# Performance work log

Hardware: AMD Instinct MI355X
Metric: run time of the kernel (lower is better)

The kernel has to match this reference:

```python
import jax, jax.numpy as jnp
import numpy as np

N_NODES = 50000
N_EDGES = 800000
F_IN, F_HID, F_OUT = 128, 256, 10


def setup_inputs() -> dict:
    key = jax.random.key(0)
    ks = jax.random.split(key, 8)
    x = jax.random.normal(ks[0], (N_NODES, F_IN), dtype=jnp.float32)
    edge_index = jax.random.randint(ks[1], (2, N_EDGES), 0, N_NODES, dtype=jnp.int64)
    # Glorot-ish init for GCNConv weights (PyG GCNConv: lin weight [in,out] + bias [out])
    def glorot(k, fi, fo):
        s = (6.0 / (fi + fo)) ** 0.5
        return jax.random.uniform(k, (fi, fo), minval=-s, maxval=s, dtype=jnp.float32)
    return {
        "x": x,
        "edge_index": edge_index,
        "W1": glorot(ks[2], F_IN, F_HID), "b1": jnp.zeros((F_HID,), jnp.float32),
        "W2": glorot(ks[3], F_HID, F_HID), "b2": jnp.zeros((F_HID,), jnp.float32),
        "W3": glorot(ks[4], F_HID, F_OUT), "b3": jnp.zeros((F_OUT,), jnp.float32),
    }


def _gcn_conv(x, W, b, src, dst, norm, n_nodes):
    # GCNConv: out[dst] += norm_e * (x @ W)[src]; then + bias
    xw = x @ W                                   # [N, F_out]
    msgs = norm[:, None] * xw[src]               # [E+N, F_out] gather
    agg = jax.ops.segment_sum(msgs, dst, num_segments=n_nodes)
    return agg + b


def reference(x, edge_index, W1, b1, W2, b2, W3, b3):
    n = x.shape[0]
    loops = jnp.arange(n, dtype=edge_index.dtype)
    src = jnp.concatenate([edge_index[0], loops])  # source nodes (messages from)
    dst = jnp.concatenate([edge_index[1], loops])  # target nodes (aggregate into)
    # symmetric normalization D^{-1/2} (A+I) D^{-1/2}, degree from target index
    deg = jax.ops.segment_sum(jnp.ones_like(dst, dtype=x.dtype), dst, num_segments=n)
    dinv = jnp.where(deg > 0, jax.lax.rsqrt(deg), 0.0)
    norm = dinv[src] * dinv[dst]

    h = _gcn_conv(x, W1, b1, src, dst, norm, n)
    h = jax.nn.relu(h)                  # dropout is identity in eval mode
    h = _gcn_conv(h, W2, b2, src, dst, norm, n)
    h = jax.nn.relu(h)
    h = _gcn_conv(h, W3, b3, src, dst, norm, n)
    return jax.nn.log_softmax(h, axis=1)
```

## Files before the change

kernel.cpp:

```cpp
#include <hip/hip_runtime.h>
#include <hip/hip_bf16.h>
#include <math.h>

#define F_IN 128
#define F_HID 256
#define F_OUT 10

typedef __attribute__((ext_vector_type(4))) short s16x4;
typedef __attribute__((ext_vector_type(8))) short s16x8;
typedef __attribute__((ext_vector_type(4))) float f32x4;

static __device__ __forceinline__ float b2f(unsigned short u) {
    union { float f; unsigned int u; } c;
    c.u = ((unsigned int)u) << 16;
    return c.f;
}
static __device__ __forceinline__ unsigned short f2b(float f) {
    return __bfloat16_as_ushort(__float2bfloat16(f));
}


__global__ void prep_kernel(const int* __restrict__ dst, int* __restrict__ cnt, int e,
                            const float* __restrict__ x, unsigned short* __restrict__ xb,
                            int xq,
                            const float* __restrict__ W1, unsigned short* __restrict__ W1t,
                            const float* __restrict__ W2, unsigned short* __restrict__ W2t) {
    int i = blockIdx.x * blockDim.x + threadIdx.x;
    int job = blockIdx.y;
    if (job == 0) {
        if (i < e) atomicAdd(&cnt[dst[i]], 1);
    } else if (job == 1) {
        if (i < xq) {
            float4 v = *(const float4*)&x[(size_t)i * 4];
            ushort4 o;
            o.x = f2b(v.x); o.y = f2b(v.y); o.z = f2b(v.z); o.w = f2b(v.w);
            *(ushort4*)&xb[(size_t)i * 4] = o;
        }
    } else if (job == 2) {
        if (i < F_IN * F_HID) {
            int k = i / F_HID, nn = i - k * F_HID;
            W1t[nn * F_IN + k] = f2b(W1[i]);
        }
    } else {
        if (i < F_HID * F_HID) {
            int k = i / F_HID, nn = i - k * F_HID;
            W2t[nn * F_HID + k] = f2b(W2[i]);
        }
    }
}


__global__ void scan1_kernel(const int* __restrict__ cnt, int* __restrict__ rowstart,
                             int* __restrict__ partial, float* __restrict__ dinv, int n) {
    __shared__ int s[256];
    int tid = threadIdx.x;
    int i = blockIdx.x * 256 + tid;
    int v = (i < n) ? cnt[i] : 0;
    s[tid] = v;
    __syncthreads();
    for (int off = 1; off < 256; off <<= 1) {
        int t = (tid >= off) ? s[tid - off] : 0;
        __syncthreads();
        s[tid] += t;
        __syncthreads();
    }
    if (i < n) {
        rowstart[i] = s[tid] - v;
        dinv[i] = rsqrtf((float)(v + 1));
    }
    if (tid == 255) partial[blockIdx.x] = s[255];
}

__global__ void scan2_kernel(int* __restrict__ partial, int nb) {
    __shared__ int s[256];
    int tid = threadIdx.x;
    int v = (tid < nb) ? partial[tid] : 0;
    s[tid] = v;
    __syncthreads();
    for (int off = 1; off < 256; off <<= 1) {
        int t = (tid >= off) ? s[tid - off] : 0;
        __syncthreads();
        s[tid] += t;
        __syncthreads();
    }
    if (tid < nb) partial[tid] = s[tid] - v;
}

__global__ void scan3_kernel(int* __restrict__ rowstart, const int* __restrict__ partial,
                             int n, int e) {
    int i = blockIdx.x * blockDim.x + threadIdx.x;
    if (i < n) rowstart[i] += partial[blockIdx.x];
    if (i == 0) rowstart[n] = e;
}

__global__ void fill_kernel(const int* __restrict__ src, const int* __restrict__ dst,
                            const int* __restrict__ rowstart, int* __restrict__ cursor,
                            const float* __restrict__ dinv, int2* __restrict__ pack, int e) {
    int i = blockIdx.x * blockDim.x + threadIdx.x;
    if (i >= e) return;
    int s = src[i], d = dst[i];
    int pos = rowstart[d] + atomicAdd(&cursor[d], 1);
    float w = dinv[s] * dinv[d];
    pack[pos] = make_int2(s, __float_as_int(w));
}


template <int F>
__global__ __launch_bounds__(256) void agg_kernel(const unsigned short* __restrict__ feat,
                                                  const int* __restrict__ rowstart,
                                                  const int2* __restrict__ pack,
                                                  const float* __restrict__ dinv,
                                                  unsigned short* __restrict__ out, int n) {
    constexpr int LPF = F / 8;
    constexpr int EG = 64 / LPF;
    int wid = threadIdx.x >> 6;
    int lane = threadIdx.x & 63;
    int v = blockIdx.x * 4 + wid;
    if (v >= n) return;
    int eg = lane / LPF;
    int fl = lane % LPF;
    const unsigned short* fp = feat + fl * 8;

    float acc[8];
    {
        float d = dinv[v];
        float sw = (eg == 0) ? d * d : 0.f;
        s16x8 t = *(const s16x8*)&fp[(size_t)v * F];
#pragma unroll
        for (int j = 0; j < 8; ++j) acc[j] = sw * b2f((unsigned short)t[j]);
    }

    int e0 = rowstart[v], e1 = rowstart[v + 1];
    constexpr int STEP = EG * 4;
    int e = e0;
    for (; e + STEP <= e1; e += STEP) {
        int2 p[4];
#pragma unroll
        for (int u = 0; u < 4; ++u) p[u] = pack[e + eg + u * EG];
        s16x8 t[4];
#pragma unroll
        for (int u = 0; u < 4; ++u) t[u] = *(const s16x8*)&fp[(size_t)p[u].x * F];
#pragma unroll
        for (int u = 0; u < 4; ++u) {
            float w = __int_as_float(p[u].y);
#pragma unroll
            for (int j = 0; j < 8; ++j) acc[j] += w * b2f((unsigned short)t[u][j]);
        }
    }
    for (int ee = e + eg; ee < e1; ee += EG) {
        int2 p = pack[ee];
        float w = __int_as_float(p.y);
        s16x8 t = *(const s16x8*)&fp[(size_t)p.x * F];
#pragma unroll
        for (int j = 0; j < 8; ++j) acc[j] += w * b2f((unsigned short)t[j]);
    }

    if (EG == 4) {
#pragma unroll
        for (int j = 0; j < 8; ++j) acc[j] += __shfl_xor(acc[j], 16);
    }
#pragma unroll
    for (int j = 0; j < 8; ++j) acc[j] += __shfl_xor(acc[j], 32);

    if (eg == 0) {
        s16x8 o;
#pragma unroll
        for (int j = 0; j < 8; ++j) o[j] = (short)f2b(acc[j]);
        *(s16x8*)&out[(size_t)v * F + fl * 8] = o;
    }
}


template <int K, bool RELU, bool BF16OUT>
__global__ __launch_bounds__(256) void gemm_mfma_kernel(const unsigned short* __restrict__ A,
                                                        const unsigned short* __restrict__ Bt,
                                                        const float* __restrict__ bias,
                                                        float* __restrict__ C,
                                                        unsigned short* __restrict__ Cb,
                                                        int M, int N) {
    __shared__ unsigned short As[64][40];
    __shared__ unsigned short Bs[64][40];
    int tid = threadIdx.x;
    int w = tid >> 6;
    int lane = tid & 63;
    int g = lane >> 4;
    int r16 = lane & 15;
    int bm = blockIdx.x, bn = blockIdx.y;

    int srow = tid >> 2;
    int scol = (tid & 3) * 8;
    int garow = bm * 64 + srow;
    int gbrow = bn * 64 + srow;

    f32x4 acc[4] = {};

    for (int k0 = 0; k0 < K; k0 += 32) {
        uint4 av = make_uint4(0, 0, 0, 0);
        if (garow < M) av = *(const uint4*)&A[(size_t)garow * K + k0 + scol];
        uint4 bv = *(const uint4*)&Bt[(size_t)gbrow * K + k0 + scol];
        __syncthreads();
        *(uint4*)&As[srow][scol] = av;
        *(uint4*)&Bs[srow][scol] = bv;
        __syncthreads();

        union U { s16x8 v; s16x4 h[2]; };
        U af;
        int arow = w * 16 + r16;
        af.h[0] = *(const s16x4*)&As[arow][g * 4];
        af.h[1] = *(const s16x4*)&As[arow][g * 4 + 16];
#pragma unroll
        for (int cg = 0; cg < 4; ++cg) {
            U bf;
            bf.h[0] = *(const s16x4*)&Bs[cg * 16 + r16][g * 4];
            bf.h[1] = *(const s16x4*)&Bs[cg * 16 + r16][g * 4 + 16];
            acc[cg] = __builtin_amdgcn_mfma_f32_16x16x32_bf16(af.v, bf.v, acc[cg], 0, 0, 0);
        }
    }

#pragma unroll
    for (int cg = 0; cg < 4; ++cg) {
        int col = bn * 64 + cg * 16 + r16;
        float bs = bias[col];
#pragma unroll
        for (int r = 0; r < 4; ++r) {
            int row = bm * 64 + w * 16 + g * 4 + r;
            if (row < M) {
                float v = acc[cg][r] + bs;
                if (RELU) v = fmaxf(v, 0.f);
                if (BF16OUT) {
                    Cb[(size_t)row * N + col] = f2b(v);
                } else {
                    C[(size_t)row * N + col] = v;
                }
            }
        }
    }
}


__global__ void gemm3_kernel(const unsigned short* __restrict__ h, const float* __restrict__ W3,
                             float* __restrict__ hw3, int M) {
    __shared__ float w[F_HID * F_OUT];
    for (int i = threadIdx.x; i < F_HID * F_OUT; i += blockDim.x) w[i] = W3[i];
    __syncthreads();
    int r = blockIdx.x * blockDim.x + threadIdx.x;
    if (r >= M) return;
    float acc[F_OUT] = {};
    const unsigned short* row = &h[(size_t)r * F_HID];
    for (int k = 0; k < F_HID; k += 8) {
        s16x8 hv = *(const s16x8*)&row[k];
#pragma unroll
        for (int u = 0; u < 8; ++u) {
            float hvf = b2f((unsigned short)hv[u]);
#pragma unroll
            for (int j = 0; j < F_OUT; ++j) acc[j] += hvf * w[(k + u) * F_OUT + j];
        }
    }
#pragma unroll
    for (int j = 0; j < F_OUT; ++j) hw3[(size_t)r * F_OUT + j] = acc[j];
}


__global__ void final_kernel(const float* __restrict__ hw3, const int* __restrict__ rowstart,
                             const int2* __restrict__ pack, const float* __restrict__ dinv,
                             const float* __restrict__ b3, float* __restrict__ out, int n) {
    int v = blockIdx.x * blockDim.x + threadIdx.x;
    if (v >= n) return;
    float acc[F_OUT];
    float d = dinv[v];
    float sw = d * d;
#pragma unroll
    for (int j = 0; j < F_OUT; ++j) acc[j] = sw * hw3[(size_t)v * F_OUT + j];
    int e0 = rowstart[v], e1 = rowstart[v + 1];
    for (int e = e0; e < e1; ++e) {
        int2 p = pack[e];
        float w = __int_as_float(p.y);
#pragma unroll
        for (int j = 0; j < F_OUT; ++j) acc[j] += w * hw3[(size_t)p.x * F_OUT + j];
    }
#pragma unroll
    for (int j = 0; j < F_OUT; ++j) acc[j] += b3[j];
    float m = acc[0];
#pragma unroll
    for (int j = 1; j < F_OUT; ++j) m = fmaxf(m, acc[j]);
    float sum = 0.f;
#pragma unroll
    for (int j = 0; j < F_OUT; ++j) sum += expf(acc[j] - m);
    float lse = m + logf(sum);
#pragma unroll
    for (int j = 0; j < F_OUT; ++j) out[(size_t)v * F_OUT + j] = acc[j] - lse;
}


extern "C" void kernel_launch(void* const* d_in, const int* in_sizes, int n_in,
                              void* d_out, int out_size, void* d_ws, size_t ws_size,
                              hipStream_t stream) {
    const float* x  = (const float*)d_in[0];
    const int*   ei = (const int*)d_in[1];
    const float* W1 = (const float*)d_in[2];
    const float* b1 = (const float*)d_in[3];
    const float* W2 = (const float*)d_in[4];
    const float* b2 = (const float*)d_in[5];
    const float* W3 = (const float*)d_in[6];
    const float* b3 = (const float*)d_in[7];
    float* out = (float*)d_out;

    int n = in_sizes[0] / F_IN;
    int e = in_sizes[1] / 2;
    const int* srcp = ei;
    const int* dstp = ei + e;

    size_t off = 0;
    auto alloc = [&](size_t bytes) -> char* {
        char* p = (char*)d_ws + off;
        off += (bytes + 255) & ~(size_t)255;
        return p;
    };
    size_t cntpad = ((size_t)n * 4 + 255) & ~(size_t)255;
    int*   cnt      = (int*)alloc((size_t)n * 4);
    int*   cursor   = (int*)alloc((size_t)n * 4);
    int*   rowstart = (int*)alloc((size_t)(n + 1) * 4);
    int*   partial  = (int*)alloc(1024 * 4);
    int2*  pack     = (int2*)alloc((size_t)e * 8);
    float* dinv     = (float*)alloc((size_t)n * 4);
    unsigned short* xb   = (unsigned short*)alloc((size_t)n * F_IN * 2);
    unsigned short* aggb = (unsigned short*)alloc((size_t)n * F_HID * 2);
    unsigned short* h1b  = (unsigned short*)alloc((size_t)n * F_HID * 2);
    unsigned short* h2b  = (unsigned short*)alloc((size_t)n * F_HID * 2);
    unsigned short* W1t  = (unsigned short*)alloc((size_t)F_IN * F_HID * 2);
    unsigned short* W2t  = (unsigned short*)alloc((size_t)F_HID * F_HID * 2);
    float* hw3 = (float*)alloc((size_t)n * F_OUT * 4);

    const int TB = 256;
    hipMemsetAsync(cnt, 0, cntpad + (size_t)n * 4, stream);

    int xq = (int)((size_t)n * F_IN / 4);
    int prepmax = e > xq ? e : xq;
    dim3 gp((prepmax + TB - 1) / TB, 4);
    prep_kernel<<<gp, TB, 0, stream>>>(dstp, cnt, e, x, xb, xq, W1, W1t, W2, W2t);

    int nb = (n + TB - 1) / TB;
    scan1_kernel<<<nb, TB, 0, stream>>>(cnt, rowstart, partial, dinv, n);
    scan2_kernel<<<1, TB, 0, stream>>>(partial, nb);
    scan3_kernel<<<nb, TB, 0, stream>>>(rowstart, partial, n, e);
    fill_kernel<<<(e + TB - 1) / TB, TB, 0, stream>>>(srcp, dstp, rowstart, cursor, dinv,
                                                      pack, e);

    int nwave = (n + 3) / 4;
    dim3 gg((n + 63) / 64, F_HID / 64);

    agg_kernel<F_IN><<<nwave, 256, 0, stream>>>(xb, rowstart, pack, dinv, aggb, n);
    gemm_mfma_kernel<F_IN, true, true><<<gg, 256, 0, stream>>>(aggb, W1t, b1, nullptr, h1b,
                                                               n, F_HID);

    agg_kernel<F_HID><<<nwave, 256, 0, stream>>>(h1b, rowstart, pack, dinv, aggb, n);
    gemm_mfma_kernel<F_HID, true, true><<<gg, 256, 0, stream>>>(aggb, W2t, b2, nullptr, h2b,
                                                                n, F_HID);

    gemm3_kernel<<<(n + TB - 1) / TB, TB, 0, stream>>>(h2b, W3, hw3, n);
    final_kernel<<<(n + TB - 1) / TB, TB, 0, stream>>>(hw3, rowstart, pack, dinv, b3, out, n);
}
```

Baseline: 269.0 us.

## Merge graph-build into cooperative kernel and fuse layer-3 GEMM into layer-2 epilogue

Replaces the memset, prep, three scan kernels and fill kernel with one cooperative kernel that uses grid syncs between phases. The MFMA GEMM now computes a full 64x256 output tile per block, so the A tile is loaded once instead of once per column block. The layer-2 GEMM epilogue applies bias and ReLU and then multiplies directly by W3, which removes the h2 intermediate buffer and the separate gemm3 kernel. In exchange, grid.sync has its own cost and the build phases run on a fixed 1024-block grid, and the larger per-block accumulator set raises register pressure, which may lower occupancy.

```diff
diff --git a/kernel.cpp b/kernel.cpp
--- a/kernel.cpp
+++ b/kernel.cpp
@@ -1,12 +1,14 @@
 #include <hip/hip_runtime.h>
+#include <hip/hip_cooperative_groups.h>
 #include <hip/hip_bf16.h>
 #include <math.h>
+
+namespace cg = cooperative_groups;
 
 #define F_IN 128
 #define F_HID 256
 #define F_OUT 10
 
-typedef __attribute__((ext_vector_type(4))) short s16x4;
 typedef __attribute__((ext_vector_type(8))) short s16x8;
 typedef __attribute__((ext_vector_type(4))) float f32x4;
 
@@ -20,88 +22,84 @@
 }
 
 
-__global__ void prep_kernel(const int* __restrict__ dst, int* __restrict__ cnt, int e,
-                            const float* __restrict__ x, unsigned short* __restrict__ xb,
-                            int xq,
-                            const float* __restrict__ W1, unsigned short* __restrict__ W1t,
-                            const float* __restrict__ W2, unsigned short* __restrict__ W2t) {
-    int i = blockIdx.x * blockDim.x + threadIdx.x;
-    int job = blockIdx.y;
-    if (job == 0) {
-        if (i < e) atomicAdd(&cnt[dst[i]], 1);
-    } else if (job == 1) {
-        if (i < xq) {
-            float4 v = *(const float4*)&x[(size_t)i * 4];
-            ushort4 o;
-            o.x = f2b(v.x); o.y = f2b(v.y); o.z = f2b(v.z); o.w = f2b(v.w);
-            *(ushort4*)&xb[(size_t)i * 4] = o;
-        }
-    } else if (job == 2) {
-        if (i < F_IN * F_HID) {
-            int k = i / F_HID, nn = i - k * F_HID;
-            W1t[nn * F_IN + k] = f2b(W1[i]);
-        }
-    } else {
-        if (i < F_HID * F_HID) {
-            int k = i / F_HID, nn = i - k * F_HID;
-            W2t[nn * F_HID + k] = f2b(W2[i]);
-        }
-    }
-}
-
-
-__global__ void scan1_kernel(const int* __restrict__ cnt, int* __restrict__ rowstart,
-                             int* __restrict__ partial, float* __restrict__ dinv, int n) {
+__global__ void __launch_bounds__(256) build_kernel(
+    const int* __restrict__ src, const int* __restrict__ dst, int e, int n,
+    const float* __restrict__ x, unsigned short* __restrict__ xb,
+    const float* __restrict__ W1, unsigned short* __restrict__ W1t,
+    const float* __restrict__ W2, unsigned short* __restrict__ W2t,
+    int* __restrict__ cnt, int* __restrict__ cursor, int* __restrict__ rowstart,
+    int* __restrict__ partial, float* __restrict__ dinv, int2* __restrict__ pack)
+{
+    cg::grid_group grid = cg::this_grid();
+    const int tid = threadIdx.x;
+    const int gtid = blockIdx.x * 256 + tid;
+    const int gs = gridDim.x * 256;
+
+    for (int i = gtid; i < n; i += gs) { cnt[i] = 0; cursor[i] = 0; }
+    const int xq = n * (F_IN / 4);
+    for (int i = gtid; i < xq; i += gs) {
+        float4 v = *(const float4*)&x[(size_t)i * 4];
+        ushort4 o;
+        o.x = f2b(v.x); o.y = f2b(v.y); o.z = f2b(v.z); o.w = f2b(v.w);
+        *(ushort4*)&xb[(size_t)i * 4] = o;
+    }
+    for (int i = gtid; i < F_IN * F_HID; i += gs) {
+        int k = i / F_HID, nn = i - k * F_HID;
+        W1t[nn * F_IN + k] = f2b(W1[i]);
+    }
+    for (int i = gtid; i < F_HID * F_HID; i += gs) {
+        int k = i / F_HID, nn = i - k * F_HID;
+        W2t[nn * F_HID + k] = f2b(W2[i]);
+    }
+    grid.sync();
+
+    for (int i = gtid; i < e; i += gs) atomicAdd(&cnt[dst[i]], 1);
+    grid.sync();
+
     __shared__ int s[256];
-    int tid = threadIdx.x;
-    int i = blockIdx.x * 256 + tid;
-    int v = (i < n) ? cnt[i] : 0;
-    s[tid] = v;
-    __syncthreads();
-    for (int off = 1; off < 256; off <<= 1) {
-        int t = (tid >= off) ? s[tid - off] : 0;
-        __syncthreads();
-        s[tid] += t;
-        __syncthreads();
-    }
-    if (i < n) {
-        rowstart[i] = s[tid] - v;
-        dinv[i] = rsqrtf((float)(v + 1));
-    }
-    if (tid == 255) partial[blockIdx.x] = s[255];
-}
-
-__global__ void scan2_kernel(int* __restrict__ partial, int nb) {
-    __shared__ int s[256];
-    int tid = threadIdx.x;
-    int v = (tid < nb) ? partial[tid] : 0;
-    s[tid] = v;
-    __syncthreads();
-    for (int off = 1; off < 256; off <<= 1) {
-        int t = (tid >= off) ? s[tid - off] : 0;
-        __syncthreads();
-        s[tid] += t;
-        __syncthreads();
-    }
-    if (tid < nb) partial[tid] = s[tid] - v;
-}
-
-__global__ void scan3_kernel(int* __restrict__ rowstart, const int* __restrict__ partial,
-                             int n, int e) {
-    int i = blockIdx.x * blockDim.x + threadIdx.x;
-    if (i < n) rowstart[i] += partial[blockIdx.x];
-    if (i == 0) rowstart[n] = e;
-}
-
-__global__ void fill_kernel(const int* __restrict__ src, const int* __restrict__ dst,
-                            const int* __restrict__ rowstart, int* __restrict__ cursor,
-                            const float* __restrict__ dinv, int2* __restrict__ pack, int e) {
-    int i = blockIdx.x * blockDim.x + threadIdx.x;
-    if (i >= e) return;
-    int s = src[i], d = dst[i];
-    int pos = rowstart[d] + atomicAdd(&cursor[d], 1);
-    float w = dinv[s] * dinv[d];
-    pack[pos] = make_int2(s, __float_as_int(w));
+    const int nb = (n + 255) >> 8;
+    if ((int)blockIdx.x < nb) {
+        int i = blockIdx.x * 256 + tid;
+        int v = (i < n) ? cnt[i] : 0;
+        s[tid] = v;
+        __syncthreads();
+        for (int o = 1; o < 256; o <<= 1) {
+            int t = (tid >= o) ? s[tid - o] : 0;
+            __syncthreads();
+            s[tid] += t;
+            __syncthreads();
+        }
+        if (i < n) rowstart[i] = s[tid] - v;
+        if (tid == 255) partial[blockIdx.x] = s[255];
+    }
+    grid.sync();
+
+    if (blockIdx.x == 0) {
+        int v = (tid < nb) ? partial[tid] : 0;
+        s[tid] = v;
+        __syncthreads();
+        for (int o = 1; o < 256; o <<= 1) {
+            int t = (tid >= o) ? s[tid - o] : 0;
+            __syncthreads();
+            s[tid] += t;
+            __syncthreads();
+        }
+        if (tid < nb) partial[tid] = s[tid] - v;
+    }
+    grid.sync();
+
+    for (int i = gtid; i < n; i += gs) {
+        rowstart[i] += partial[i >> 8];
+        dinv[i] = rsqrtf((float)(cnt[i] + 1));
+    }
+    if (gtid == 0) rowstart[n] = e;
+    grid.sync();
+
+    for (int i = gtid; i < e; i += gs) {
+        int ss = src[i], d = dst[i];
+        int pos = rowstart[d] + atomicAdd(&cursor[d], 1);
+        pack[pos] = make_int2(ss, __float_as_int(dinv[ss] * dinv[d]));
+    }
 }
 
 
@@ -171,93 +169,100 @@
 }
 
 
-template <int K, bool RELU, bool BF16OUT>
-__global__ __launch_bounds__(256) void gemm_mfma_kernel(const unsigned short* __restrict__ A,
-                                                        const unsigned short* __restrict__ Bt,
-                                                        const float* __restrict__ bias,
-                                                        float* __restrict__ C,
-                                                        unsigned short* __restrict__ Cb,
-                                                        int M, int N) {
+template <int K, bool FUSE3>
+__global__ __launch_bounds__(256) void gemm_kernel(const unsigned short* __restrict__ A,
+                                                   const unsigned short* __restrict__ Bt,
+                                                   const float* __restrict__ bias,
+                                                   unsigned short* __restrict__ Cb,
+                                                   const float* __restrict__ W3,
+                                                   float* __restrict__ hw3, int M) {
+    constexpr int N = F_HID;
     __shared__ unsigned short As[64][40];
-    __shared__ unsigned short Bs[64][40];
-    int tid = threadIdx.x;
-    int w = tid >> 6;
-    int lane = tid & 63;
-    int g = lane >> 4;
-    int r16 = lane & 15;
-    int bm = blockIdx.x, bn = blockIdx.y;
-
-    int srow = tid >> 2;
-    int scol = (tid & 3) * 8;
-    int garow = bm * 64 + srow;
-    int gbrow = bn * 64 + srow;
-
-    f32x4 acc[4] = {};
+    __shared__ unsigned short Bs[N][40];
+    const int tid = threadIdx.x;
+    const int w = tid >> 6, lane = tid & 63;
+    const int g = lane >> 4, r16 = lane & 15;
+    const int bm = blockIdx.x;
+
+    const int sArow = tid >> 2;
+    const int sAkq = (tid & 3) * 8;
+    const int garow = bm * 64 + sArow;
+
+    f32x4 acc[16] = {};
 
     for (int k0 = 0; k0 < K; k0 += 32) {
         uint4 av = make_uint4(0, 0, 0, 0);
-        if (garow < M) av = *(const uint4*)&A[(size_t)garow * K + k0 + scol];
-        uint4 bv = *(const uint4*)&Bt[(size_t)gbrow * K + k0 + scol];
-        __syncthreads();
-        *(uint4*)&As[srow][scol] = av;
-        *(uint4*)&Bs[srow][scol] = bv;
-        __syncthreads();
-
-        union U { s16x8 v; s16x4 h[2]; };
-        U af;
-        int arow = w * 16 + r16;
-        af.h[0] = *(const s16x4*)&As[arow][g * 4];
-        af.h[1] = *(const s16x4*)&As[arow][g * 4 + 16];
-#pragma unroll
-        for (int cg = 0; cg < 4; ++cg) {
-            U bf;
-            bf.h[0] = *(const s16x4*)&Bs[cg * 16 + r16][g * 4];
-            bf.h[1] = *(const s16x4*)&Bs[cg * 16 + r16][g * 4 + 16];
-            acc[cg] = __builtin_amdgcn_mfma_f32_16x16x32_bf16(af.v, bf.v, acc[cg], 0, 0, 0);
-        }
-    }
-
-#pragma unroll
-    for (int cg = 0; cg < 4; ++cg) {
-        int col = bn * 64 + cg * 16 + r16;
-        float bs = bias[col];
-#pragma unroll
-        for (int r = 0; r < 4; ++r) {
-            int row = bm * 64 + w * 16 + g * 4 + r;
-            if (row < M) {
-                float v = acc[cg][r] + bs;
-                if (RELU) v = fmaxf(v, 0.f);
-                if (BF16OUT) {
+        if (garow < M) av = *(const uint4*)&A[(size_t)garow * K + k0 + sAkq];
+        uint4 bv0 = *(const uint4*)&Bt[(size_t)tid * K + k0 + 0];
+        uint4 bv1 = *(const uint4*)&Bt[(size_t)tid * K + k0 + 8];
+        uint4 bv2 = *(const uint4*)&Bt[(size_t)tid * K + k0 + 16];
+        uint4 bv3 = *(const uint4*)&Bt[(size_t)tid * K + k0 + 24];
+        __syncthreads();
+        *(uint4*)&As[sArow][sAkq] = av;
+        *(uint4*)&Bs[tid][0] = bv0;
+        *(uint4*)&Bs[tid][8] = bv1;
+        *(uint4*)&Bs[tid][16] = bv2;
+        *(uint4*)&Bs[tid][24] = bv3;
+        __syncthreads();
+
+        s16x8 af = *(const s16x8*)&As[w * 16 + r16][g * 8];
+#pragma unroll
+        for (int cg = 0; cg < 16; ++cg) {
+            s16x8 bf = *(const s16x8*)&Bs[cg * 16 + r16][g * 8];
+            acc[cg] = __builtin_amdgcn_mfma_f32_16x16x32_bf16(af, bf, acc[cg], 0, 0, 0);
+        }
+    }
+
+    if constexpr (!FUSE3) {
+#pragma unroll
+        for (int cg = 0; cg < 16; ++cg) {
+            int col = cg * 16 + r16;
+            float bs = bias[col];
+#pragma unroll
+            for (int r = 0; r < 4; ++r) {
+                int row = bm * 64 + w * 16 + g * 4 + r;
+                if (row < M) {
+                    float v = fmaxf(acc[cg][r] + bs, 0.f);
                     Cb[(size_t)row * N + col] = f2b(v);
-                } else {
-                    C[(size_t)row * N + col] = v;
                 }
             }
         }
-    }
-}
-
-
-__global__ void gemm3_kernel(const unsigned short* __restrict__ h, const float* __restrict__ W3,
-                             float* __restrict__ hw3, int M) {
-    __shared__ float w[F_HID * F_OUT];
-    for (int i = threadIdx.x; i < F_HID * F_OUT; i += blockDim.x) w[i] = W3[i];
-    __syncthreads();
-    int r = blockIdx.x * blockDim.x + threadIdx.x;
-    if (r >= M) return;
-    float acc[F_OUT] = {};
-    const unsigned short* row = &h[(size_t)r * F_HID];
-    for (int k = 0; k < F_HID; k += 8) {
-        s16x8 hv = *(const s16x8*)&row[k];
-#pragma unroll
-        for (int u = 0; u < 8; ++u) {
-            float hvf = b2f((unsigned short)hv[u]);
-#pragma unroll
-            for (int j = 0; j < F_OUT; ++j) acc[j] += hvf * w[(k + u) * F_OUT + j];
-        }
-    }
-#pragma unroll
-    for (int j = 0; j < F_OUT; ++j) hw3[(size_t)r * F_OUT + j] = acc[j];
+    } else {
+        float* W3s = (float*)&Bs[0][0];
+        __syncthreads();
+        for (int i = tid; i < N * F_OUT; i += 256) W3s[i] = W3[i];
+        __syncthreads();
+
+        float bcol[16];
+#pragma unroll
+        for (int cg = 0; cg < 16; ++cg) bcol[cg] = bias[cg * 16 + r16];
+
+#pragma unroll
+        for (int r = 0; r < 4; ++r) {
+            float pj[F_OUT] = {};
+#pragma unroll
+            for (int cg = 0; cg < 16; ++cg) {
+                float v = fmaxf(acc[cg][r] + bcol[cg], 0.f);
+                const float* w3r = &W3s[(cg * 16 + r16) * F_OUT];
+#pragma unroll
+                for (int j = 0; j < F_OUT; ++j) pj[j] += v * w3r[j];
+            }
+#pragma unroll
+            for (int j = 0; j < F_OUT; ++j) {
+                pj[j] += __shfl_xor(pj[j], 1);
+                pj[j] += __shfl_xor(pj[j], 2);
+                pj[j] += __shfl_xor(pj[j], 4);
+                pj[j] += __shfl_xor(pj[j], 8);
+            }
+            if (r16 == 0) {
+                int row = bm * 64 + w * 16 + g * 4 + r;
+                if (row < M) {
+#pragma unroll
+                    for (int j = 0; j < F_OUT; ++j) hw3[(size_t)row * F_OUT + j] = pj[j];
+                }
+            }
+        }
+    }
 }
 
 
@@ -316,7 +321,6 @@
         off += (bytes + 255) & ~(size_t)255;
         return p;
     };
-    size_t cntpad = ((size_t)n * 4 + 255) & ~(size_t)255;
     int*   cnt      = (int*)alloc((size_t)n * 4);
     int*   cursor   = (int*)alloc((size_t)n * 4);
     int*   rowstart = (int*)alloc((size_t)(n + 1) * 4);
@@ -326,37 +330,23 @@
     unsigned short* xb   = (unsigned short*)alloc((size_t)n * F_IN * 2);
     unsigned short* aggb = (unsigned short*)alloc((size_t)n * F_HID * 2);
     unsigned short* h1b  = (unsigned short*)alloc((size_t)n * F_HID * 2);
-    unsigned short* h2b  = (unsigned short*)alloc((size_t)n * F_HID * 2);
     unsigned short* W1t  = (unsigned short*)alloc((size_t)F_IN * F_HID * 2);
     unsigned short* W2t  = (unsigned short*)alloc((size_t)F_HID * F_HID * 2);
     float* hw3 = (float*)alloc((size_t)n * F_OUT * 4);
 
-    const int TB = 256;
-    hipMemsetAsync(cnt, 0, cntpad + (size_t)n * 4, stream);
-
-    int xq = (int)((size_t)n * F_IN / 4);
-    int prepmax = e > xq ? e : xq;
-    dim3 gp((prepmax + TB - 1) / TB, 4);
-    prep_kernel<<<gp, TB, 0, stream>>>(dstp, cnt, e, x, xb, xq, W1, W1t, W2, W2t);
-
-    int nb = (n + TB - 1) / TB;
-    scan1_kernel<<<nb, TB, 0, stream>>>(cnt, rowstart, partial, dinv, n);
-    scan2_kernel<<<1, TB, 0, stream>>>(partial, nb);
-    scan3_kernel<<<nb, TB, 0, stream>>>(rowstart, partial, n, e);
-    fill_kernel<<<(e + TB - 1) / TB, TB, 0, stream>>>(srcp, dstp, rowstart, cursor, dinv,
-                                                      pack, e);
+    void* args[] = { (void*)&srcp, (void*)&dstp, (void*)&e, (void*)&n,
+                     (void*)&x, (void*)&xb, (void*)&W1, (void*)&W1t,
+                     (void*)&W2, (void*)&W2t,
+                     (void*)&cnt, (void*)&cursor, (void*)&rowstart,
+                     (void*)&partial, (void*)&dinv, (void*)&pack };
+    hipLaunchCooperativeKernel((void*)build_kernel, dim3(1024), dim3(256), args, 0, stream);
 
     int nwave = (n + 3) / 4;
-    dim3 gg((n + 63) / 64, F_HID / 64);
+    int gblocks = (n + 63) / 64;
 
     agg_kernel<F_IN><<<nwave, 256, 0, stream>>>(xb, rowstart, pack, dinv, aggb, n);
-    gemm_mfma_kernel<F_IN, true, true><<<gg, 256, 0, stream>>>(aggb, W1t, b1, nullptr, h1b,
-                                                               n, F_HID);
-
+    gemm_kernel<F_IN, false><<<gblocks, 256, 0, stream>>>(aggb, W1t, b1, h1b, nullptr, nullptr, n);
     agg_kernel<F_HID><<<nwave, 256, 0, stream>>>(h1b, rowstart, pack, dinv, aggb, n);
-    gemm_mfma_kernel<F_HID, true, true><<<gg, 256, 0, stream>>>(aggb, W2t, b2, nullptr, h2b,
-                                                                n, F_HID);
-
-    gemm3_kernel<<<(n + TB - 1) / TB, TB, 0, stream>>>(h2b, W3, hw3, n);
-    final_kernel<<<(n + TB - 1) / TB, TB, 0, stream>>>(hw3, rowstart, pack, dinv, b3, out, n);
-}
+    gemm_kernel<F_HID, true><<<gblocks, 256, 0, stream>>>(aggb, W2t, b2, nullptr, W3, hw3, n);
+    final_kernel<<<(n + 255) / 256, 256, 0, stream>>>(hw3, rowstart, pack, dinv, b3, out, n);
+}
```

After: 760.1 us. +182.5%, slower.
